# Kernel tuning notes

Measured on AMD Instinct MI355X. Metric: run time of the kernel, lower is better.

## Reference

```python
import jax, jax.numpy as jnp
import numpy as np

# Model dims (DeepSeek-V2-lite style MLA)
B, T, DIM = 1, 2048, 2048
H = 16
NOPE, ROPE, VD = 128, 64, 128
QKD = NOPE + ROPE            # 192
Q_LORA, KV_LORA = 768, 512
EPS = 1e-6
SOFTSCALE = QKD * -0.5       # faithful to source: qk_head_dim * -0.5 == -96.0 (NOT **-0.5)


def rms_norm(x, w):
    # F.rms_norm: x / sqrt(mean(x^2) + eps) * w
    return x * jax.lax.rsqrt(jnp.mean(x * x, axis=-1, keepdims=True) + EPS) * w


def apply_rope(x, freqs):
    # x: [B, T, H, D] with D even; freqs: [T, D//2] rotation angles.
    # Complex-pair rotation on interleaved (even, odd) pairs, DeepSeek style.
    b, t, h, d = x.shape
    xr = x.reshape(b, t, h, d // 2, 2)
    cos = jnp.cos(freqs)[None, :, None, :]
    sin = jnp.sin(freqs)[None, :, None, :]
    x1, x2 = xr[..., 0], xr[..., 1]
    out = jnp.stack([x1 * cos - x2 * sin, x1 * sin + x2 * cos], axis=-1)
    return out.reshape(b, t, h, d)


def setup_inputs() -> dict:
    key = jax.random.key(0)
    ks = jax.random.split(key, 8)

    def w(k, out_f, in_f):
        return jax.random.normal(k, (out_f, in_f), dtype=jnp.float32) * (in_f ** -0.5)

    x = jax.random.normal(ks[0], (B, T, DIM), dtype=jnp.float32)

    # RoPE angles: positions x inv_freq, [T, ROPE//2]
    inv_freq = 1.0 / (10000.0 ** (np.arange(0, ROPE, 2, dtype=np.float32) / ROPE))
    freqs = jnp.asarray(np.outer(np.arange(T, dtype=np.float32), inv_freq))

    # additive causal mask [T, T]
    mask = jnp.where(np.tril(np.ones((T, T), dtype=bool)), 0.0, -jnp.inf).astype(jnp.float32)

    return {
        "x": x,
        "freqs": freqs,
        "mask": mask,
        "wq_a": w(ks[1], Q_LORA, DIM),
        "q_norm_w": jnp.ones((Q_LORA,), dtype=jnp.float32),
        "wq_b": w(ks[2], H * QKD, Q_LORA),
        "wkv_a": w(ks[3], KV_LORA + ROPE, DIM),
        "kv_norm_w": jnp.ones((KV_LORA,), dtype=jnp.float32),
        "wkv_b": w(ks[4], H * (NOPE + VD), KV_LORA),
        "wo": w(ks[5], DIM, H * VD),
    }


def reference(x, freqs, mask, wq_a, q_norm_w, wq_b, wkv_a, kv_norm_w, wkv_b, wo):
    b, t, _ = x.shape

    # low-rank query path: wq_b(rms_norm(wq_a(x)))
    q = rms_norm(x @ wq_a.T, q_norm_w) @ wq_b.T            # [B,T,H*QKD]
    q = q.reshape(b, t, H, QKD)
    q_nope, q_pe = q[..., :NOPE], q[..., NOPE:]
    q_pe = apply_rope(q_pe, freqs)

    # low-rank kv path
    kv_full = x @ wkv_a.T                                  # [B,T,KV_LORA+ROPE]
    c_kv, k_pe = kv_full[..., :KV_LORA], kv_full[..., KV_LORA:]
    k_pe = apply_rope(k_pe[:, :, None, :], freqs)          # [B,T,1,ROPE]
    kv = rms_norm(c_kv, kv_norm_w) @ wkv_b.T               # [B,T,H*(NOPE+VD)]
    kv = kv.reshape(b, t, H, NOPE + VD)
    k_nope, v = kv[..., :NOPE], kv[..., NOPE:]

    qh = jnp.concatenate([q_nope, q_pe], axis=-1)          # [B,T,H,QKD]
    kh = jnp.concatenate([k_nope, jnp.broadcast_to(k_pe, (b, t, H, ROPE))], axis=-1)

    # scores [B,S,H,T]; mask.unsqueeze(1) in torch -> mask[:, None, :] here
    scores = jnp.einsum("bshd,bthd->bsht", qh, kh) * SOFTSCALE
    scores = scores + mask[:, None, :]
    attn = jax.nn.softmax(scores.astype(jnp.float32), axis=-1).astype(x.dtype)

    y = jnp.einsum("bsht,bthd->bshd", attn, v)             # [B,T,H,VD]
    out = y.reshape(b, t, H * VD) @ wo.T                   # [B,T,DIM]
    return out
```

## Files before the change

kernel.cpp:

```cpp
#include <hip/hip_runtime.h>
#include <hip/hip_bf16.h>
#include <math.h>


#define T_DIM 2048
#define HEADS 16
#define D_MODEL 2048
#define NOPE_D 128
#define ROPE_D 64
#define QKD_D 192
#define VD_D 128
#define QLORA 768
#define KVLORA 512
#define KVFULL_D 576
#define SOFTSCALE -96.0f
#define EPS_RMS 1e-6f

typedef __hip_bfloat16 bf;
typedef __attribute__((ext_vector_type(8))) short bf16x8;
typedef __attribute__((ext_vector_type(4))) float f32x4;

#define GLOAD_LDS16(gptr, lptr)                                               \
    __builtin_amdgcn_global_load_lds(                                         \
        (const __attribute__((address_space(1))) unsigned int*)(gptr),        \
        (__attribute__((address_space(3))) unsigned int*)(lptr), 16, 0, 0)

__device__ __forceinline__ void split2(float v, bf* hi, bf* lo) {
    bf h = __float2bfloat16(v);
    *hi = h;
    *lo = __float2bfloat16(v - __bfloat162float(h));
}

__global__ __launch_bounds__(256) void cvt_split(
    const float* __restrict__ in, bf* __restrict__ hi, bf* __restrict__ lo, int n)
{
    const int i = (blockIdx.x * 256 + threadIdx.x) * 4;
    if (i >= n) return;
    float4 v = *(const float4*)&in[i];
    float vv[4] = {v.x, v.y, v.z, v.w};
#pragma unroll
    for (int u = 0; u < 4; u++) split2(vv[u], &hi[i + u], &lo[i + u]);
}

__global__ __launch_bounds__(256) void rmsnorm_cvt(
    const float* __restrict__ in, int ld, int D, const float* __restrict__ w,
    bf* __restrict__ hi, bf* __restrict__ lo)
{
    const int row = blockIdx.x;
    const float* r = in + (size_t)row * ld;
    float ss = 0.0f;
    for (int i = threadIdx.x; i < D; i += 256) { float v = r[i]; ss += v * v; }
#pragma unroll
    for (int o = 32; o > 0; o >>= 1) ss += __shfl_down(ss, o, 64);
    __shared__ float red[4];
    if ((threadIdx.x & 63) == 0) red[threadIdx.x >> 6] = ss;
    __syncthreads();
    ss = red[0] + red[1] + red[2] + red[3];
    const float scale = rsqrtf(ss / (float)D + EPS_RMS);
    for (int i = threadIdx.x; i < D; i += 256) {
        const float v = r[i] * scale * w[i];
        split2(v, &hi[(size_t)row * D + i], &lo[(size_t)row * D + i]);
    }
}

__global__ __launch_bounds__(256) void rope_k_cvt(
    const float* __restrict__ kvfull, const float* __restrict__ freqs,
    bf* __restrict__ kpeh, bf* __restrict__ kpel)
{
    const int idx = blockIdx.x * 256 + threadIdx.x;
    const int i = idx & 31, t = idx >> 5;
    const float f = freqs[t * 32 + i];
    float sn, cs; sincosf(f, &sn, &cs);
    const float x1 = kvfull[(size_t)t * KVFULL_D + KVLORA + 2 * i];
    const float x2 = kvfull[(size_t)t * KVFULL_D + KVLORA + 2 * i + 1];
    split2(x1 * cs - x2 * sn, &kpeh[t * 64 + 2 * i], &kpel[t * 64 + 2 * i]);
    split2(x1 * sn + x2 * cs, &kpeh[t * 64 + 2 * i + 1], &kpel[t * 64 + 2 * i + 1]);
}

__global__ __launch_bounds__(256) void transpose_v(
    const bf* __restrict__ vh, bf* __restrict__ vT)
{
    __shared__ bf s[32][33];
    const int t0 = blockIdx.x * 32, d0 = blockIdx.y * 32, h = blockIdx.z;
    const int tid = threadIdx.x;
    const int i = tid >> 3, j0 = (tid & 7) * 4;
    const bf* src = vh + ((size_t)(t0 + i) * 16 + h) * 128 + d0 + j0;
#pragma unroll
    for (int u = 0; u < 4; u++) s[i][j0 + u] = src[u];
    __syncthreads();
    const int jj = tid >> 3, i0 = (tid & 7) * 4;
    bf* dst = vT + ((size_t)h * 128 + d0 + jj) * 2048 + t0 + i0;
#pragma unroll
    for (int u = 0; u < 4; u++) dst[u] = s[i0 + u][jj];
}

template <int MODE>
__global__ __launch_bounds__(256) void gemm_split(
    const bf* __restrict__ Ah, const bf* __restrict__ Al,
    const bf* __restrict__ Bh, const bf* __restrict__ Bl,
    const float* __restrict__ freqs,
    float* __restrict__ Cf, bf* __restrict__ Oh, bf* __restrict__ Ol,
    bf* __restrict__ O2, int M, int N, int K)
{
    __shared__ bf sAh[128 * 32], sAl[128 * 32];
    __shared__ bf sBh[128 * 32], sBl[128 * 32];

    const int tid = threadIdx.x;
    const int lane = tid & 63, wave = tid >> 6;
    const int row0 = blockIdx.y * 128, col0 = blockIdx.x * 128;
    const int wm = (wave & 1) * 64, wn = (wave >> 1) * 64;
    const int fr = lane & 15, quad = lane >> 4;

    f32x4 acc[4][4];
#pragma unroll
    for (int i = 0; i < 4; i++)
#pragma unroll
        for (int j = 0; j < 4; j++) acc[i][j] = (f32x4){0.f, 0.f, 0.f, 0.f};

    const int trow = tid >> 2;
    const int tcol = (tid & 3) * 8;
    const size_t ldsoff = (size_t)wave * 1024;
    int br0 = col0 + trow;      if (br0 > N - 1) br0 = N - 1;
    int br1 = col0 + 64 + trow; if (br1 > N - 1) br1 = N - 1;

    for (int kt = 0; kt < K; kt += 32) {
        __syncthreads();
        GLOAD_LDS16(Ah + (size_t)(row0 + trow) * K + kt + tcol,      (char*)sAh + ldsoff);
        GLOAD_LDS16(Ah + (size_t)(row0 + 64 + trow) * K + kt + tcol, (char*)sAh + 4096 + ldsoff);
        GLOAD_LDS16(Al + (size_t)(row0 + trow) * K + kt + tcol,      (char*)sAl + ldsoff);
        GLOAD_LDS16(Al + (size_t)(row0 + 64 + trow) * K + kt + tcol, (char*)sAl + 4096 + ldsoff);
        GLOAD_LDS16(Bh + (size_t)br0 * K + kt + tcol, (char*)sBh + ldsoff);
        GLOAD_LDS16(Bh + (size_t)br1 * K + kt + tcol, (char*)sBh + 4096 + ldsoff);
        GLOAD_LDS16(Bl + (size_t)br0 * K + kt + tcol, (char*)sBl + ldsoff);
        GLOAD_LDS16(Bl + (size_t)br1 * K + kt + tcol, (char*)sBl + 4096 + ldsoff);
        __syncthreads();

        bf16x8 a_h[4], a_l[4], b_h[4], b_l[4];
#pragma unroll
        for (int mt = 0; mt < 4; mt++) {
            const int r = (wm + mt * 16 + fr) * 32 + quad * 8;
            a_h[mt] = *(const bf16x8*)&sAh[r];
            a_l[mt] = *(const bf16x8*)&sAl[r];
        }
#pragma unroll
        for (int nt = 0; nt < 4; nt++) {
            const int r = (wn + nt * 16 + fr) * 32 + quad * 8;
            b_h[nt] = *(const bf16x8*)&sBh[r];
            b_l[nt] = *(const bf16x8*)&sBl[r];
        }
#pragma unroll
        for (int mt = 0; mt < 4; mt++)
#pragma unroll
            for (int nt = 0; nt < 4; nt++) {
                acc[mt][nt] = __builtin_amdgcn_mfma_f32_16x16x32_bf16(
                    a_l[mt], b_h[nt], acc[mt][nt], 0, 0, 0);
                acc[mt][nt] = __builtin_amdgcn_mfma_f32_16x16x32_bf16(
                    a_h[mt], b_l[nt], acc[mt][nt], 0, 0, 0);
                acc[mt][nt] = __builtin_amdgcn_mfma_f32_16x16x32_bf16(
                    a_h[mt], b_h[nt], acc[mt][nt], 0, 0, 0);
            }
    }

#pragma unroll
    for (int mt = 0; mt < 4; mt++)
#pragma unroll
        for (int nt = 0; nt < 4; nt++) {
            const int colb = col0 + wn + nt * 16;
            const int col = colb + fr;
            if (MODE == 0) {
#pragma unroll
                for (int r = 0; r < 4; r++) {
                    const int row = row0 + wm + mt * 16 + quad * 4 + r;
                    if (col < N) Cf[(size_t)row * N + col] = acc[mt][nt][r];
                }
            } else if (MODE == 1) {
                const int d0 = colb % 192;
                const bool rope = (d0 >= 128);
                const int ii = (d0 + fr - 128) >> 1;
#pragma unroll
                for (int r = 0; r < 4; r++) {
                    const int row = row0 + wm + mt * 16 + quad * 4 + r;
                    float v = acc[mt][nt][r];
                    if (rope) {
                        const float other = __shfl_xor(v, 1);
                        float sn, cs; sincosf(freqs[row * 32 + ii], &sn, &cs);
                        v = (fr & 1) ? (other * sn + v * cs) : (v * cs - other * sn);
                    }
                    bf h8, l8; split2(v, &h8, &l8);
                    Oh[(size_t)row * N + col] = h8;
                    Ol[(size_t)row * N + col] = l8;
                }
            } else {
                const int hh = col >> 8;
                const int d = col & 255;
#pragma unroll
                for (int r = 0; r < 4; r++) {
                    const int row = row0 + wm + mt * 16 + quad * 4 + r;
                    const float v = acc[mt][nt][r];
                    if (d < 128) {
                        bf h8, l8; split2(v, &h8, &l8);
                        Oh[(size_t)row * 2048 + hh * 128 + d] = h8;
                        Ol[(size_t)row * 2048 + hh * 128 + d] = l8;
                    } else {
                        O2[(size_t)row * 2048 + hh * 128 + (d - 128)] = __float2bfloat16(v);
                    }
                }
            }
        }
}

__global__ __launch_bounds__(256, 2) void attn_mfma(
    const bf* __restrict__ qh, const bf* __restrict__ ql,
    const bf* __restrict__ knh, const bf* __restrict__ knl,
    const bf* __restrict__ kpeh, const bf* __restrict__ kpel,
    const bf* __restrict__ vT,
    bf* __restrict__ yh, bf* __restrict__ yl)
{
    const int bid = blockIdx.x;
    const int h = bid & 15;
    const int qt = (bid < 256) ? (31 - (bid >> 4)) : ((bid - 256) >> 4);
    const int tid = threadIdx.x;
    const int lane = tid & 63, wave = tid >> 6;
    const int fr = lane & 15, quad = lane >> 4;
    const int wn = wave * 32;

    __shared__ bf sQh[64 * 32], sQl[64 * 32];
    __shared__ bf sKh[128 * 32], sKl[128 * 32];
    __shared__ bf Ps[64 * 128];
    __shared__ bf sVt[128 * 32];
    __shared__ float redM[64][4];
    __shared__ float redS[64][4];

    float m_i[16], l_i[16];
    f32x4 O[4][2];
#pragma unroll
    for (int i = 0; i < 16; i++) { m_i[i] = -INFINITY; l_i[i] = 0.0f; }
#pragma unroll
    for (int mt = 0; mt < 4; mt++)
#pragma unroll
        for (int nt = 0; nt < 2; nt++) O[mt][nt] = (f32x4){0.f, 0.f, 0.f, 0.f};

    const int q0 = qt * 64;
    const int nkt = (64 * qt + 191) >> 7;
    const int trow = tid >> 2, tcol = (tid & 3) * 8;
    const size_t loff = (size_t)wave * 1024;

    for (int kt = 0; kt < nkt; kt++) {
        const int k0 = kt * 128;
        f32x4 S[4][2];
#pragma unroll
        for (int mt = 0; mt < 4; mt++)
#pragma unroll
            for (int nt = 0; nt < 2; nt++) S[mt][nt] = (f32x4){0.f, 0.f, 0.f, 0.f};

        for (int ch = 0; ch < 6; ch++) {
            const int d0 = ch * 32;
            __syncthreads();
            GLOAD_LDS16(qh + ((size_t)(q0 + trow) * 16 + h) * 192 + d0 + tcol, (char*)sQh + loff);
            GLOAD_LDS16(ql + ((size_t)(q0 + trow) * 16 + h) * 192 + d0 + tcol, (char*)sQl + loff);
            if (d0 < 128) {
                GLOAD_LDS16(knh + ((size_t)(k0 + trow) * 16 + h) * 128 + d0 + tcol,      (char*)sKh + loff);
                GLOAD_LDS16(knh + ((size_t)(k0 + 64 + trow) * 16 + h) * 128 + d0 + tcol, (char*)sKh + 4096 + loff);
                GLOAD_LDS16(knl + ((size_t)(k0 + trow) * 16 + h) * 128 + d0 + tcol,      (char*)sKl + loff);
                GLOAD_LDS16(knl + ((size_t)(k0 + 64 + trow) * 16 + h) * 128 + d0 + tcol, (char*)sKl + 4096 + loff);
            } else {
                GLOAD_LDS16(kpeh + (size_t)(k0 + trow) * 64 + (d0 - 128) + tcol,      (char*)sKh + loff);
                GLOAD_LDS16(kpeh + (size_t)(k0 + 64 + trow) * 64 + (d0 - 128) + tcol, (char*)sKh + 4096 + loff);
                GLOAD_LDS16(kpel + (size_t)(k0 + trow) * 64 + (d0 - 128) + tcol,      (char*)sKl + loff);
                GLOAD_LDS16(kpel + (size_t)(k0 + 64 + trow) * 64 + (d0 - 128) + tcol, (char*)sKl + 4096 + loff);
            }
            __syncthreads();

            bf16x8 a_h[4], a_l[4], b_h[2], b_l[2];
#pragma unroll
            for (int mt = 0; mt < 4; mt++) {
                const int r = (mt * 16 + fr) * 32 + quad * 8;
                a_h[mt] = *(const bf16x8*)&sQh[r];
                a_l[mt] = *(const bf16x8*)&sQl[r];
            }
#pragma unroll
            for (int nt = 0; nt < 2; nt++) {
                const int r = (wn + nt * 16 + fr) * 32 + quad * 8;
                b_h[nt] = *(const bf16x8*)&sKh[r];
                b_l[nt] = *(const bf16x8*)&sKl[r];
            }
#pragma unroll
            for (int mt = 0; mt < 4; mt++)
#pragma unroll
                for (int nt = 0; nt < 2; nt++) {
                    S[mt][nt] = __builtin_amdgcn_mfma_f32_16x16x32_bf16(
                        a_l[mt], b_h[nt], S[mt][nt], 0, 0, 0);
                    S[mt][nt] = __builtin_amdgcn_mfma_f32_16x16x32_bf16(
                        a_h[mt], b_l[nt], S[mt][nt], 0, 0, 0);
                    S[mt][nt] = __builtin_amdgcn_mfma_f32_16x16x32_bf16(
                        a_h[mt], b_h[nt], S[mt][nt], 0, 0, 0);
                }
        }

        float al[16];
#pragma unroll
        for (int mt = 0; mt < 4; mt++)
#pragma unroll
            for (int rr = 0; rr < 4; rr++) {
                const int ri = mt * 16 + quad * 4 + rr;
                const int rowg = q0 + ri;
                float v0 = S[mt][0][rr] * SOFTSCALE;
                float v1 = S[mt][1][rr] * SOFTSCALE;
                if (k0 + wn + fr > rowg)      v0 = -INFINITY;
                if (k0 + wn + 16 + fr > rowg) v1 = -INFINITY;
                S[mt][0][rr] = v0; S[mt][1][rr] = v1;
                float pm = fmaxf(v0, v1);
#pragma unroll
                for (int o = 1; o < 16; o <<= 1) pm = fmaxf(pm, __shfl_xor(pm, o, 64));
                if (fr == 0) redM[ri][wave] = pm;
            }
        __syncthreads();
#pragma unroll
        for (int mt = 0; mt < 4; mt++)
#pragma unroll
            for (int rr = 0; rr < 4; rr++) {
                const int idx = mt * 4 + rr;
                const int ri = mt * 16 + quad * 4 + rr;
                const float4 g = *(const float4*)&redM[ri][0];
                const float gm = fmaxf(fmaxf(g.x, g.y), fmaxf(g.z, g.w));
                const float mn = fmaxf(m_i[idx], gm);
                al[idx] = __expf(m_i[idx] - mn);
                m_i[idx] = mn;
            }
#pragma unroll
        for (int mt = 0; mt < 4; mt++)
#pragma unroll
            for (int rr = 0; rr < 4; rr++) {
                const int idx = mt * 4 + rr;
                const int ri = mt * 16 + quad * 4 + rr;
                const float p0 = __expf(S[mt][0][rr] - m_i[idx]);
                const float p1 = __expf(S[mt][1][rr] - m_i[idx]);
                Ps[ri * 128 + wn + fr]      = __float2bfloat16(p0);
                Ps[ri * 128 + wn + 16 + fr] = __float2bfloat16(p1);
                float ps = p0 + p1;
#pragma unroll
                for (int o = 1; o < 16; o <<= 1) ps += __shfl_xor(ps, o, 64);
                if (fr == 0) redS[ri][wave] = ps;
            }
#pragma unroll
        for (int mt = 0; mt < 4; mt++)
#pragma unroll
            for (int nt = 0; nt < 2; nt++)
#pragma unroll
                for (int rr = 0; rr < 4; rr++) O[mt][nt][rr] *= al[mt * 4 + rr];
        __syncthreads();
#pragma unroll
        for (int mt = 0; mt < 4; mt++)
#pragma unroll
            for (int rr = 0; rr < 4; rr++) {
                const int idx = mt * 4 + rr;
                const int ri = mt * 16 + quad * 4 + rr;
                const float4 s4 = *(const float4*)&redS[ri][0];
                l_i[idx] = l_i[idx] * al[idx] + (s4.x + s4.y + s4.z + s4.w);
            }

        for (int vch = 0; vch < 4; vch++) {
            if (vch) __syncthreads();
            GLOAD_LDS16(vT + ((size_t)(h * 128 + trow)) * 2048 + k0 + vch * 32 + tcol,      (char*)sVt + loff);
            GLOAD_LDS16(vT + ((size_t)(h * 128 + 64 + trow)) * 2048 + k0 + vch * 32 + tcol, (char*)sVt + 4096 + loff);
            __syncthreads();
            bf16x8 ap[4], bv[2];
#pragma unroll
            for (int mt = 0; mt < 4; mt++)
                ap[mt] = *(const bf16x8*)&Ps[(mt * 16 + fr) * 128 + vch * 32 + quad * 8];
#pragma unroll
            for (int nt = 0; nt < 2; nt++)
                bv[nt] = *(const bf16x8*)&sVt[(wn + nt * 16 + fr) * 32 + quad * 8];
#pragma unroll
            for (int mt = 0; mt < 4; mt++)
#pragma unroll
                for (int nt = 0; nt < 2; nt++)
                    O[mt][nt] = __builtin_amdgcn_mfma_f32_16x16x32_bf16(
                        ap[mt], bv[nt], O[mt][nt], 0, 0, 0);
        }
    }

#pragma unroll
    for (int mt = 0; mt < 4; mt++)
#pragma unroll
        for (int rr = 0; rr < 4; rr++) {
            const float inv = 1.0f / l_i[mt * 4 + rr];
            const int row = q0 + mt * 16 + quad * 4 + rr;
#pragma unroll
            for (int nt = 0; nt < 2; nt++) {
                const int col = wn + nt * 16 + fr;
                const float v = O[mt][nt][rr] * inv;
                bf h8, l8; split2(v, &h8, &l8);
                yh[((size_t)row * 16 + h) * 128 + col] = h8;
                yl[((size_t)row * 16 + h) * 128 + col] = l8;
            }
        }
}

extern "C" void kernel_launch(void* const* d_in, const int* in_sizes, int n_in,
                              void* d_out, int out_size, void* d_ws, size_t ws_size,
                              hipStream_t stream)
{
    const float* x        = (const float*)d_in[0];
    const float* freqs    = (const float*)d_in[1];
    const float* wq_a     = (const float*)d_in[3];
    const float* q_norm_w = (const float*)d_in[4];
    const float* wq_b     = (const float*)d_in[5];
    const float* wkv_a    = (const float*)d_in[6];
    const float* kv_norm_w= (const float*)d_in[7];
    const float* wkv_b    = (const float*)d_in[8];
    const float* wo       = (const float*)d_in[9];
    float* out            = (float*)d_out;

    char* ws = (char*)d_ws;
    bf* xh = (bf*)(ws);
    bf* xl = (bf*)(ws + 8388608);
    bf* yh = (bf*)(ws);
    bf* yl = (bf*)(ws + 8388608);
    char* AR = ws + 16777216;
    bf*    wah    = (bf*)(AR);
    bf*    wal    = (bf*)(AR + 3145728);
    float* qa     = (float*)(AR + 6291456);
    bf*    qah    = (bf*)(AR);
    bf*    qal    = (bf*)(AR + 3145728);
    bf*    wbh    = (bf*)(AR + 6291456);
    bf*    wbl    = (bf*)(AR + 11010048);
    bf*    kah    = (bf*)(AR);
    bf*    kal    = (bf*)(AR + 2359296);
    float* kvfull = (float*)(AR + 4718592);
    bf*    ckvh   = (bf*)(AR + 9437184);
    bf*    ckvl   = (bf*)(AR + 11534336);
    bf*    wvh    = (bf*)(AR);
    bf*    wvl    = (bf*)(AR + 4194304);
    bf*    vT     = (bf*)(AR);
    bf*    woh    = (bf*)(AR);
    bf*    wol    = (bf*)(AR + 8388608);
    bf* qh   = (bf*)(ws + 33554432);
    bf* ql   = (bf*)(ws + 46137344);
    bf* knh  = (bf*)(ws + 58720256);
    bf* knl  = (bf*)(ws + 67108864);
    bf* vh   = (bf*)(ws + 75497472);
    bf* kpeh = (bf*)(ws + 83886080);
    bf* kpel = (bf*)(ws + 84148224);

    dim3 blk(256);

    cvt_split<<<4096, blk, 0, stream>>>(x, xh, xl, D_MODEL * D_MODEL);
    cvt_split<<<1536, blk, 0, stream>>>(wq_a, wah, wal, QLORA * D_MODEL);
    gemm_split<0><<<dim3(6, 16), blk, 0, stream>>>(
        xh, xl, wah, wal, nullptr, qa, nullptr, nullptr, nullptr,
        T_DIM, QLORA, D_MODEL);
    rmsnorm_cvt<<<T_DIM, blk, 0, stream>>>(qa, QLORA, QLORA, q_norm_w, qah, qal);
    cvt_split<<<2304, blk, 0, stream>>>(wq_b, wbh, wbl, 3072 * QLORA);
    gemm_split<1><<<dim3(24, 16), blk, 0, stream>>>(
        qah, qal, wbh, wbl, freqs, nullptr, qh, ql, nullptr,
        T_DIM, 3072, QLORA);
    cvt_split<<<1152, blk, 0, stream>>>(wkv_a, kah, kal, KVFULL_D * D_MODEL);
    gemm_split<0><<<dim3(5, 16), blk, 0, stream>>>(
        xh, xl, kah, kal, nullptr, kvfull, nullptr, nullptr, nullptr,
        T_DIM, KVFULL_D, D_MODEL);
    rope_k_cvt<<<256, blk, 0, stream>>>(kvfull, freqs, kpeh, kpel);
    rmsnorm_cvt<<<T_DIM, blk, 0, stream>>>(kvfull, KVFULL_D, KVLORA, kv_norm_w, ckvh, ckvl);
    cvt_split<<<2048, blk, 0, stream>>>(wkv_b, wvh, wvl, 4096 * KVLORA);
    gemm_split<2><<<dim3(32, 16), blk, 0, stream>>>(
        ckvh, ckvl, wvh, wvl, nullptr, nullptr, knh, knl, vh,
        T_DIM, 4096, KVLORA);
    transpose_v<<<dim3(64, 4, 16), blk, 0, stream>>>(vh, vT);
    attn_mfma<<<dim3(512), blk, 0, stream>>>(
        qh, ql, knh, knl, kpeh, kpel, vT, yh, yl);
    cvt_split<<<4096, blk, 0, stream>>>(wo, woh, wol, D_MODEL * D_MODEL);
    gemm_split<0><<<dim3(16, 16), blk, 0, stream>>>(
        yh, yl, woh, wol, nullptr, out, nullptr, nullptr, nullptr,
        T_DIM, D_MODEL, D_MODEL);
}
```

Baseline: 720.0 us.

## Split attention KV range across blocks with merge pass; use single-bf16 output projection

Attention is split along the key dimension into 512-key slices, launching 1280 blocks instead of 512. Each block writes partial O, m and l to workspace, and a new merge kernel combines them, which balances the causal workload and raises parallelism. Shared memory is reduced and aliased so the occupancy hint rises to 4 blocks per CU, and P is written in 64-column halves. The output projection drops the hi/lo split and uses a plain bf16 GEMM. That removes one weight-split pass and two-thirds of its MFMAs, at the cost of precision, and the partial O is also stored in bf16.

After: 1.160 ms. 1.61x slower.

```diff
diff --git a/kernel.cpp b/kernel.cpp
--- a/kernel.cpp
+++ b/kernel.cpp
@@ -20,6 +20,9 @@
 typedef __attribute__((ext_vector_type(8))) short bf16x8;
 typedef __attribute__((ext_vector_type(4))) float f32x4;
 
+#define SLICE_BYTES 16896
+#define PART1_CAP 992
+
 #define GLOAD_LDS16(gptr, lptr)                                               \
     __builtin_amdgcn_global_load_lds(                                         \
         (const __attribute__((address_space(1))) unsigned int*)(gptr),        \
@@ -40,6 +43,18 @@
     float vv[4] = {v.x, v.y, v.z, v.w};
 #pragma unroll
     for (int u = 0; u < 4; u++) split2(vv[u], &hi[i + u], &lo[i + u]);
+}
+
+__global__ __launch_bounds__(256) void cvt_hi(
+    const float* __restrict__ in, bf* __restrict__ hi, int n)
+{
+    const int i = (blockIdx.x * 256 + threadIdx.x) * 4;
+    if (i >= n) return;
+    float4 v = *(const float4*)&in[i];
+    hi[i + 0] = __float2bfloat16(v.x);
+    hi[i + 1] = __float2bfloat16(v.y);
+    hi[i + 2] = __float2bfloat16(v.z);
+    hi[i + 3] = __float2bfloat16(v.w);
 }
 
 __global__ __launch_bounds__(256) void rmsnorm_cvt(
@@ -209,29 +224,94 @@
         }
 }
 
-__global__ __launch_bounds__(256, 2) void attn_mfma(
+__global__ __launch_bounds__(256) void gemm_bf16(
+    const bf* __restrict__ Ah, const bf* __restrict__ Bh,
+    float* __restrict__ Cf, int M, int N, int K)
+{
+    __shared__ bf sAh[128 * 32];
+    __shared__ bf sBh[128 * 32];
+
+    const int tid = threadIdx.x;
+    const int lane = tid & 63, wave = tid >> 6;
+    const int row0 = blockIdx.y * 128, col0 = blockIdx.x * 128;
+    const int wm = (wave & 1) * 64, wn = (wave >> 1) * 64;
+    const int fr = lane & 15, quad = lane >> 4;
+
+    f32x4 acc[4][4];
+#pragma unroll
+    for (int i = 0; i < 4; i++)
+#pragma unroll
+        for (int j = 0; j < 4; j++) acc[i][j] = (f32x4){0.f, 0.f, 0.f, 0.f};
+
+    const int trow = tid >> 2;
+    const int tcol = (tid & 3) * 8;
+    const size_t ldsoff = (size_t)wave * 1024;
+
+    for (int kt = 0; kt < K; kt += 32) {
+        __syncthreads();
+        GLOAD_LDS16(Ah + (size_t)(row0 + trow) * K + kt + tcol,      (char*)sAh + ldsoff);
+        GLOAD_LDS16(Ah + (size_t)(row0 + 64 + trow) * K + kt + tcol, (char*)sAh + 4096 + ldsoff);
+        GLOAD_LDS16(Bh + (size_t)(col0 + trow) * K + kt + tcol,      (char*)sBh + ldsoff);
+        GLOAD_LDS16(Bh + (size_t)(col0 + 64 + trow) * K + kt + tcol, (char*)sBh + 4096 + ldsoff);
+        __syncthreads();
+
+        bf16x8 a_h[4], b_h[4];
+#pragma unroll
+        for (int mt = 0; mt < 4; mt++)
+            a_h[mt] = *(const bf16x8*)&sAh[(wm + mt * 16 + fr) * 32 + quad * 8];
+#pragma unroll
+        for (int nt = 0; nt < 4; nt++)
+            b_h[nt] = *(const bf16x8*)&sBh[(wn + nt * 16 + fr) * 32 + quad * 8];
+#pragma unroll
+        for (int mt = 0; mt < 4; mt++)
+#pragma unroll
+            for (int nt = 0; nt < 4; nt++)
+                acc[mt][nt] = __builtin_amdgcn_mfma_f32_16x16x32_bf16(
+                    a_h[mt], b_h[nt], acc[mt][nt], 0, 0, 0);
+    }
+
+#pragma unroll
+    for (int mt = 0; mt < 4; mt++)
+#pragma unroll
+        for (int nt = 0; nt < 4; nt++)
+#pragma unroll
+            for (int r = 0; r < 4; r++)
+                Cf[(size_t)(row0 + wm + mt * 16 + quad * 4 + r) * N +
+                   col0 + wn + nt * 16 + fr] = acc[mt][nt][r];
+}
+
+__global__ __launch_bounds__(256, 4) void attn_mfma(
     const bf* __restrict__ qh, const bf* __restrict__ ql,
     const bf* __restrict__ knh, const bf* __restrict__ knl,
     const bf* __restrict__ kpeh, const bf* __restrict__ kpel,
     const bf* __restrict__ vT,
-    bf* __restrict__ yh, bf* __restrict__ yl)
+    char* __restrict__ part1, char* __restrict__ part2)
 {
     const int bid = blockIdx.x;
     const int h = bid & 15;
-    const int qt = (bid < 256) ? (31 - (bid >> 4)) : ((bid - 256) >> 4);
+    const int sidx = bid >> 4;
+    int qt, s;
+    if (sidx < 8)       { qt = sidx; s = 0; }
+    else if (sidx < 24) { const int r = sidx - 8;  qt = 8  + (r >> 1); s = r & 1; }
+    else if (sidx < 48) { const int r = sidx - 24; qt = 16 + r / 3;    s = r % 3; }
+    else                { const int r = sidx - 48; qt = 24 + (r >> 2); s = r & 3; }
+
     const int tid = threadIdx.x;
     const int lane = tid & 63, wave = tid >> 6;
     const int fr = lane & 15, quad = lane >> 4;
     const int wn = wave * 32;
 
-    __shared__ bf sQh[64 * 32], sQl[64 * 32];
-    __shared__ bf sKh[128 * 32], sKl[128 * 32];
-    __shared__ bf Ps[64 * 128];
-    __shared__ bf sVt[128 * 32];
-    __shared__ float redM[64][4];
-    __shared__ float redS[64][4];
-
-    float m_i[16], l_i[16];
+    __shared__ __align__(16) char smem[35840];
+    bf* sQh = (bf*)(smem);
+    bf* sQl = (bf*)(smem + 4096);
+    bf* sKh = (bf*)(smem + 8192);
+    bf* sKl = (bf*)(smem + 16384);
+    bf* sVt = (bf*)(smem + 8192);
+    bf* Ps  = (bf*)(smem + 24576);
+    float* redM = (float*)(smem + 33792);
+    float* redS = (float*)(smem + 34816);
+
+    float m_i[16], l_i[16], al[16];
     f32x4 O[4][2];
 #pragma unroll
     for (int i = 0; i < 16; i++) { m_i[i] = -INFINITY; l_i[i] = 0.0f; }
@@ -241,12 +321,12 @@
         for (int nt = 0; nt < 2; nt++) O[mt][nt] = (f32x4){0.f, 0.f, 0.f, 0.f};
 
     const int q0 = qt * 64;
-    const int nkt = (64 * qt + 191) >> 7;
+    const int kstart = s * 512;
+    const int kend = min(kstart + 512, (qt + 1) * 64);
     const int trow = tid >> 2, tcol = (tid & 3) * 8;
     const size_t loff = (size_t)wave * 1024;
 
-    for (int kt = 0; kt < nkt; kt++) {
-        const int k0 = kt * 128;
+    for (int k0 = kstart; k0 < kend; k0 += 128) {
         f32x4 S[4][2];
 #pragma unroll
         for (int mt = 0; mt < 4; mt++)
@@ -297,7 +377,6 @@
                 }
         }
 
-        float al[16];
 #pragma unroll
         for (int mt = 0; mt < 4; mt++)
 #pragma unroll
@@ -312,7 +391,7 @@
                 float pm = fmaxf(v0, v1);
 #pragma unroll
                 for (int o = 1; o < 16; o <<= 1) pm = fmaxf(pm, __shfl_xor(pm, o, 64));
-                if (fr == 0) redM[ri][wave] = pm;
+                if (fr == 0) redM[ri * 4 + wave] = pm;
             }
         __syncthreads();
 #pragma unroll
@@ -321,80 +400,136 @@
             for (int rr = 0; rr < 4; rr++) {
                 const int idx = mt * 4 + rr;
                 const int ri = mt * 16 + quad * 4 + rr;
-                const float4 g = *(const float4*)&redM[ri][0];
+                const float4 g = *(const float4*)&redM[ri * 4];
                 const float gm = fmaxf(fmaxf(g.x, g.y), fmaxf(g.z, g.w));
                 const float mn = fmaxf(m_i[idx], gm);
                 al[idx] = __expf(m_i[idx] - mn);
                 m_i[idx] = mn;
-            }
+                const float p0 = __expf(S[mt][0][rr] - mn);
+                const float p1 = __expf(S[mt][1][rr] - mn);
+                float ps = p0 + p1;
+#pragma unroll
+                for (int o = 1; o < 16; o <<= 1) ps += __shfl_xor(ps, o, 64);
+                if (fr == 0) redS[ri * 4 + wave] = ps;
+            }
+#pragma unroll
+        for (int mt = 0; mt < 4; mt++)
+#pragma unroll
+            for (int nt = 0; nt < 2; nt++)
+#pragma unroll
+                for (int rr = 0; rr < 4; rr++) O[mt][nt][rr] *= al[mt * 4 + rr];
+        __syncthreads();
 #pragma unroll
         for (int mt = 0; mt < 4; mt++)
 #pragma unroll
             for (int rr = 0; rr < 4; rr++) {
                 const int idx = mt * 4 + rr;
                 const int ri = mt * 16 + quad * 4 + rr;
-                const float p0 = __expf(S[mt][0][rr] - m_i[idx]);
-                const float p1 = __expf(S[mt][1][rr] - m_i[idx]);
-                Ps[ri * 128 + wn + fr]      = __float2bfloat16(p0);
-                Ps[ri * 128 + wn + 16 + fr] = __float2bfloat16(p1);
-                float ps = p0 + p1;
-#pragma unroll
-                for (int o = 1; o < 16; o <<= 1) ps += __shfl_xor(ps, o, 64);
-                if (fr == 0) redS[ri][wave] = ps;
-            }
-#pragma unroll
-        for (int mt = 0; mt < 4; mt++)
-#pragma unroll
-            for (int nt = 0; nt < 2; nt++)
-#pragma unroll
-                for (int rr = 0; rr < 4; rr++) O[mt][nt][rr] *= al[mt * 4 + rr];
-        __syncthreads();
-#pragma unroll
-        for (int mt = 0; mt < 4; mt++)
-#pragma unroll
-            for (int rr = 0; rr < 4; rr++) {
-                const int idx = mt * 4 + rr;
-                const int ri = mt * 16 + quad * 4 + rr;
-                const float4 s4 = *(const float4*)&redS[ri][0];
+                const float4 s4 = *(const float4*)&redS[ri * 4];
                 l_i[idx] = l_i[idx] * al[idx] + (s4.x + s4.y + s4.z + s4.w);
             }
 
-        for (int vch = 0; vch < 4; vch++) {
-            if (vch) __syncthreads();
-            GLOAD_LDS16(vT + ((size_t)(h * 128 + trow)) * 2048 + k0 + vch * 32 + tcol,      (char*)sVt + loff);
-            GLOAD_LDS16(vT + ((size_t)(h * 128 + 64 + trow)) * 2048 + k0 + vch * 32 + tcol, (char*)sVt + 4096 + loff);
-            __syncthreads();
-            bf16x8 ap[4], bv[2];
-#pragma unroll
-            for (int mt = 0; mt < 4; mt++)
-                ap[mt] = *(const bf16x8*)&Ps[(mt * 16 + fr) * 128 + vch * 32 + quad * 8];
-#pragma unroll
-            for (int nt = 0; nt < 2; nt++)
-                bv[nt] = *(const bf16x8*)&sVt[(wn + nt * 16 + fr) * 32 + quad * 8];
-#pragma unroll
-            for (int mt = 0; mt < 4; mt++)
+#pragma unroll
+        for (int half = 0; half < 2; half++) {
+            if ((wave >> 1) == half) {
+                const int kc = wn - half * 64;
+#pragma unroll
+                for (int mt = 0; mt < 4; mt++)
+#pragma unroll
+                    for (int rr = 0; rr < 4; rr++) {
+                        const int idx = mt * 4 + rr;
+                        const int ri = mt * 16 + quad * 4 + rr;
+                        Ps[ri * 72 + kc + fr]      = __float2bfloat16(__expf(S[mt][0][rr] - m_i[idx]));
+                        Ps[ri * 72 + kc + 16 + fr] = __float2bfloat16(__expf(S[mt][1][rr] - m_i[idx]));
+                    }
+            }
+#pragma unroll
+            for (int vc = 0; vc < 2; vc++) {
+                const int kb = k0 + half * 64 + vc * 32;
+                GLOAD_LDS16(vT + ((size_t)(h * 128 + trow)) * 2048 + kb + tcol,      (char*)sVt + loff);
+                GLOAD_LDS16(vT + ((size_t)(h * 128 + 64 + trow)) * 2048 + kb + tcol, (char*)sVt + 4096 + loff);
+                __syncthreads();
+                bf16x8 ap[4], bv[2];
+#pragma unroll
+                for (int mt = 0; mt < 4; mt++)
+                    ap[mt] = *(const bf16x8*)&Ps[(mt * 16 + fr) * 72 + vc * 32 + quad * 8];
 #pragma unroll
                 for (int nt = 0; nt < 2; nt++)
-                    O[mt][nt] = __builtin_amdgcn_mfma_f32_16x16x32_bf16(
-                        ap[mt], bv[nt], O[mt][nt], 0, 0, 0);
+                    bv[nt] = *(const bf16x8*)&sVt[(wn + nt * 16 + fr) * 32 + quad * 8];
+#pragma unroll
+                for (int mt = 0; mt < 4; mt++)
+#pragma unroll
+                    for (int nt = 0; nt < 2; nt++)
+                        O[mt][nt] = __builtin_amdgcn_mfma_f32_16x16x32_bf16(
+                            ap[mt], bv[nt], O[mt][nt], 0, 0, 0);
+                __syncthreads();
+            }
         }
     }
 
+    const int g = h * 80 + sidx;
+    char* base = (g < PART1_CAP) ? part1 + (size_t)g * SLICE_BYTES
+                                 : part2 + (size_t)(g - PART1_CAP) * SLICE_BYTES;
+    bf* Op = (bf*)base;
+    float* mp = (float*)(base + 16384);
+    float* lp = (float*)(base + 16640);
 #pragma unroll
     for (int mt = 0; mt < 4; mt++)
 #pragma unroll
         for (int rr = 0; rr < 4; rr++) {
-            const float inv = 1.0f / l_i[mt * 4 + rr];
-            const int row = q0 + mt * 16 + quad * 4 + rr;
-#pragma unroll
-            for (int nt = 0; nt < 2; nt++) {
-                const int col = wn + nt * 16 + fr;
-                const float v = O[mt][nt][rr] * inv;
-                bf h8, l8; split2(v, &h8, &l8);
-                yh[((size_t)row * 16 + h) * 128 + col] = h8;
-                yl[((size_t)row * 16 + h) * 128 + col] = l8;
-            }
+            const int idx = mt * 4 + rr;
+            const int ri = mt * 16 + quad * 4 + rr;
+#pragma unroll
+            for (int nt = 0; nt < 2; nt++)
+                Op[ri * 128 + wn + nt * 16 + fr] = __float2bfloat16(O[mt][nt][rr]);
+            if (wave == 0 && fr == 0) { mp[ri] = m_i[idx]; lp[ri] = l_i[idx]; }
         }
+}
+
+__global__ __launch_bounds__(256) void attn_merge(
+    const char* __restrict__ part1, const char* __restrict__ part2,
+    bf* __restrict__ yh)
+{
+    const int h = blockIdx.x & 15, qt = blockIdx.x >> 4;
+    const int a = qt >> 3, b = qt & 7;
+    const int sidx0 = 4 * a * (a + 1) + b * (a + 1);
+    const int nst = a + 1;
+    const int tid = threadIdx.x;
+    const int r = tid >> 2;
+    const int c0 = (tid & 3) * 32;
+
+    const char* bases[4];
+    float m_s[4], l_s[4];
+    for (int s = 0; s < nst; s++) {
+        const int g = h * 80 + sidx0 + s;
+        bases[s] = (g < PART1_CAP) ? part1 + (size_t)g * SLICE_BYTES
+                                   : part2 + (size_t)(g - PART1_CAP) * SLICE_BYTES;
+        m_s[s] = ((const float*)(bases[s] + 16384))[r];
+        l_s[s] = ((const float*)(bases[s] + 16640))[r];
+    }
+    float M = -INFINITY;
+    for (int s = 0; s < nst; s++) M = fmaxf(M, m_s[s]);
+    float denom = 0.0f;
+    for (int s = 0; s < nst; s++) denom += __expf(m_s[s] - M) * l_s[s];
+    float w[4];
+    for (int s = 0; s < nst; s++) w[s] = __expf(m_s[s] - M) / denom;
+
+    const int row = qt * 64 + r;
+    bf* dst = yh + ((size_t)row * 16 + h) * 128 + c0;
+#pragma unroll
+    for (int cc = 0; cc < 32; cc += 8) {
+        float acc[8] = {0, 0, 0, 0, 0, 0, 0, 0};
+        for (int s = 0; s < nst; s++) {
+            const bf16x8 ov = *(const bf16x8*)((const bf*)bases[s] + r * 128 + c0 + cc);
+#pragma unroll
+            for (int u = 0; u < 8; u++) {
+                union { short s16; bf b16; } cv; cv.s16 = ov[u];
+                acc[u] += w[s] * __bfloat162float(cv.b16);
+            }
+        }
+#pragma unroll
+        for (int u = 0; u < 8; u++) dst[cc + u] = __float2bfloat16(acc[u]);
+    }
 }
 
 extern "C" void kernel_launch(void* const* d_in, const int* in_sizes, int n_in,
@@ -416,7 +551,7 @@
     bf* xh = (bf*)(ws);
     bf* xl = (bf*)(ws + 8388608);
     bf* yh = (bf*)(ws);
-    bf* yl = (bf*)(ws + 8388608);
+    bf* vT = (bf*)(ws + 8388608);
     char* AR = ws + 16777216;
     bf*    wah    = (bf*)(AR);
     bf*    wal    = (bf*)(AR + 3145728);
@@ -432,14 +567,14 @@
     bf*    ckvl   = (bf*)(AR + 11534336);
     bf*    wvh    = (bf*)(AR);
     bf*    wvl    = (bf*)(AR + 4194304);
-    bf*    vT     = (bf*)(AR);
+    char*  part1  = AR;
     bf*    woh    = (bf*)(AR);
-    bf*    wol    = (bf*)(AR + 8388608);
     bf* qh   = (bf*)(ws + 33554432);
     bf* ql   = (bf*)(ws + 46137344);
     bf* knh  = (bf*)(ws + 58720256);
     bf* knl  = (bf*)(ws + 67108864);
     bf* vh   = (bf*)(ws + 75497472);
+    char* part2 = ws + 75497472;
     bf* kpeh = (bf*)(ws + 83886080);
     bf* kpel = (bf*)(ws + 84148224);
 
@@ -466,10 +601,10 @@
         ckvh, ckvl, wvh, wvl, nullptr, nullptr, knh, knl, vh,
         T_DIM, 4096, KVLORA);
     transpose_v<<<dim3(64, 4, 16), blk, 0, stream>>>(vh, vT);
-    attn_mfma<<<dim3(512), blk, 0, stream>>>(
-        qh, ql, knh, knl, kpeh, kpel, vT, yh, yl);
-    cvt_split<<<4096, blk, 0, stream>>>(wo, woh, wol, D_MODEL * D_MODEL);
-    gemm_split<0><<<dim3(16, 16), blk, 0, stream>>>(
-        yh, yl, woh, wol, nullptr, out, nullptr, nullptr, nullptr,
-        T_DIM, D_MODEL, D_MODEL);
-}
+    attn_mfma<<<dim3(1280), blk, 0, stream>>>(
+        qh, ql, knh, knl, kpeh, kpel, vT, part1, part2);
+    attn_merge<<<dim3(512), blk, 0, stream>>>(part1, part2, yh);
+    cvt_hi<<<4096, blk, 0, stream>>>(wo, woh, D_MODEL * D_MODEL);
+    gemm_bf16<<<dim3(16, 16), blk, 0, stream>>>(
+        yh, woh, out, T_DIM, D_MODEL, D_MODEL);
+}
```
